# Kernel optimization log

Measured on AMD Instinct MI355X. Metric: run time of the kernel, lower is better.

## Reference

```python
import jax, jax.numpy as jnp
import numpy as np

N = 50000
E = 800000
D_IN = 256
D_H = 256


def setup_inputs() -> dict:
    key = jax.random.key(0)
    ks = jax.random.split(key, 8)
    x = jax.random.normal(ks[0], (N, D_IN), dtype=jnp.float32)
    W1 = jax.random.normal(ks[1], (D_H, D_IN), dtype=jnp.float32) * (1.0 / np.sqrt(D_IN))
    b1 = jnp.zeros((D_H,), dtype=jnp.float32)
    W2 = jax.random.normal(ks[2], (D_H, D_H), dtype=jnp.float32) * (1.0 / np.sqrt(D_H))
    b2 = jnp.zeros((D_H,), dtype=jnp.float32)
    gamma = jnp.ones((D_H,), dtype=jnp.float32)
    beta = jnp.zeros((D_H,), dtype=jnp.float32)
    adj_values = jax.random.uniform(ks[3], (E,), dtype=jnp.float32)
    rows = jax.random.randint(ks[4], (E,), 0, N, dtype=jnp.int64)
    cols = jax.random.randint(ks[5], (E,), 0, N, dtype=jnp.int64)
    adj_indices = jnp.stack([rows, cols], axis=0)
    return {"x": x, "W1": W1, "b1": b1, "W2": W2, "b2": b2,
            "gamma": gamma, "beta": beta, "adj_values": adj_values,
            "adj_indices": adj_indices}


def _spmm(adj_indices, adj_values, h, n):
    # out[i] = sum_j A[i, j] * h[j]; COO row=indices[0], col=indices[1]
    rows, cols = adj_indices[0], adj_indices[1]
    msgs = adj_values[:, None] * h[cols]          # [E, D]
    return jax.ops.segment_sum(msgs, rows, num_segments=n)


def _layernorm(h, gamma, beta, eps=1e-5):
    mu = jnp.mean(h, axis=-1, keepdims=True)
    var = jnp.var(h, axis=-1, keepdims=True)
    return (h - mu) * jax.lax.rsqrt(var + eps) * gamma + beta


def reference(x, W1, b1, W2, b2, gamma, beta, adj_values, adj_indices):
    n = x.shape[0]
    h = x @ W1.T + b1
    h = _spmm(adj_indices, adj_values, h, n)
    h = jax.nn.gelu(h, approximate=False)
    h = h @ W2.T + b2
    h = _spmm(adj_indices, adj_values, h, n)
    h = jax.nn.gelu(h, approximate=False)
    h = _layernorm(h + x[:, :h.shape[1]], gamma, beta)
    return h
```

## Files before the change

### kernel.cpp

```cpp
#include <hip/hip_runtime.h>
#include <math.h>

#define DH 256
#define CAP 64

typedef _Float16 f16x4 __attribute__((ext_vector_type(4)));
typedef _Float16 f16x8 __attribute__((ext_vector_type(8)));
typedef __fp16 fp16x2 __attribute__((ext_vector_type(2)));
typedef float f32x4 __attribute__((ext_vector_type(4)));

__device__ __forceinline__ float gelu_exact(float v) {
    return 0.5f * v * (1.0f + erff(v * 0.70710678118654752f));
}

__device__ __forceinline__ unsigned short f2h_bits(float f) {
    _Float16 h = (_Float16)f;
    return __builtin_bit_cast(unsigned short, h);
}

__device__ __forceinline__ _Float16 bits2h(unsigned short u) {
    return __builtin_bit_cast(_Float16, u);
}

__device__ __forceinline__ unsigned pk2h(float a, float b) {
    fp16x2 r = __builtin_amdgcn_cvt_pkrtz(a, b);
    return __builtin_bit_cast(unsigned, r);
}

__device__ __forceinline__ void async_copy16(const void* g, void* l) {
    __builtin_amdgcn_global_load_lds(
        (const __attribute__((address_space(1))) void*)g,
        (__attribute__((address_space(3))) void*)l, 16, 0, 0);
}

__global__ void prep_kernel(const float* __restrict__ W1, const float* __restrict__ W2,
                            unsigned short* __restrict__ W1h, unsigned short* __restrict__ W2h,
                            int* __restrict__ cnt, int n) {
    const int WV = DH * DH / 4;
    int gid = blockIdx.x * blockDim.x + threadIdx.x;
    if (gid < 2 * WV) {
        const float* src = (gid < WV) ? W1 : W2;
        unsigned short* dst = (gid < WV) ? W1h : W2h;
        int i = (gid < WV) ? gid : gid - WV;
        float4 v = *(const float4*)(src + (size_t)i * 4);
        uint2 o;
        o.x = pk2h(v.x, v.y);
        o.y = pk2h(v.z, v.w);
        *(uint2*)(dst + (size_t)i * 4) = o;
    } else {
        int i = (gid - 2 * WV) * 4;
        if (i < n) {
            int4 z = {0, 0, 0, 0};
            if (i + 4 <= n) *(int4*)(cnt + i) = z;
            else for (int k = i; k < n; ++k) cnt[k] = 0;
        }
    }
}

__global__ void bucket_kernel(const int* __restrict__ idx, const float* __restrict__ vals,
                              int* __restrict__ cnt, unsigned* __restrict__ cvb, int E) {
    int e = blockIdx.x * blockDim.x + threadIdx.x;
    if (e >= E) return;
    int r = idx[e];
    int c = idx[E + e];
    float v = vals[e];
    int p = atomicAdd(&cnt[r], 1);
    if (p < CAP) {
        cvb[(size_t)r * CAP + p] = ((unsigned)c << 16) | (unsigned)f2h_bits(v);
    }
}

template<bool AF32>
__global__ __launch_bounds__(512) void gemm_mfma_kernel(
        const void* __restrict__ Ap, const unsigned short* __restrict__ B,
        const float* __restrict__ bias, unsigned short* __restrict__ C, int M) {
    __shared__ char smem[49152];
    char* sA = smem;
    char* sB = smem + 16384;
    const int tid  = threadIdx.x;
    const int lane = tid & 63;
    const int wid  = tid >> 6;
    const int m0   = blockIdx.x * 128;
    const int wm   = wid >> 2;
    const int wn   = wid & 3;
    const int l15  = lane & 15, l4 = lane >> 4;

    auto stage = [&](int k0) {
        #pragma unroll
        for (int k = 0; k < 2; ++k) {
            int t = k * 512 + tid;
            int row = t >> 3;
            int sw  = (t & 7) ^ (row & 7);
            int gra = m0 + row; if (gra >= M) gra = M - 1;
            if (AF32) {
                const float* a32 = (const float*)Ap + (size_t)gra * DH + k0 + sw * 8;
                float4 lo = *(const float4*)a32;
                float4 hi = *(const float4*)(a32 + 4);
                uint4 pk;
                pk.x = pk2h(lo.x, lo.y);
                pk.y = pk2h(lo.z, lo.w);
                pk.z = pk2h(hi.x, hi.y);
                pk.w = pk2h(hi.z, hi.w);
                *(uint4*)(sA + (size_t)t * 16) = pk;
            } else {
                async_copy16((const unsigned short*)Ap + (size_t)gra * DH + k0 + sw * 8,
                             sA + ((size_t)(k * 512 + wid * 64)) * 16);
            }
        }
        #pragma unroll
        for (int k = 0; k < 4; ++k) {
            int t = k * 512 + tid;
            int row = t >> 3;
            int sw  = (t & 7) ^ (row & 7);
            async_copy16(B + (size_t)row * DH + k0 + sw * 8,
                         sB + ((size_t)(k * 512 + wid * 64)) * 16);
        }
    };

    f32x4 acc[4][4] = {};

    stage(0);
    __syncthreads();

    #pragma unroll
    for (int t = 0; t < 4; ++t) {
        f16x8 af[4][2], bfg[4][2];
        #pragma unroll
        for (int f = 0; f < 4; ++f) {
            int ra = wm * 64 + f * 16 + l15;
            int rb = wn * 64 + f * 16 + l15;
            #pragma unroll
            for (int kf = 0; kf < 2; ++kf) {
                int ca = ((kf * 4 + l4) ^ (ra & 7)) * 16;
                int cb = ((kf * 4 + l4) ^ (rb & 7)) * 16;
                af[f][kf]  = *(const f16x8*)(sA + ra * 128 + ca);
                bfg[f][kf] = *(const f16x8*)(sB + rb * 128 + cb);
            }
        }
        #pragma unroll
        for (int fm = 0; fm < 4; ++fm)
            #pragma unroll
            for (int fn = 0; fn < 4; ++fn) {
                acc[fm][fn] = __builtin_amdgcn_mfma_f32_16x16x32_f16(af[fm][0], bfg[fn][0], acc[fm][fn], 0, 0, 0);
                acc[fm][fn] = __builtin_amdgcn_mfma_f32_16x16x32_f16(af[fm][1], bfg[fn][1], acc[fm][fn], 0, 0, 0);
            }
        if (t < 3) {
            __syncthreads();
            stage((t + 1) * 64);
            __syncthreads();
        }
    }

    #pragma unroll
    for (int fn = 0; fn < 4; ++fn) {
        float bb = bias[wn * 64 + fn * 16 + l15];
        #pragma unroll
        for (int fm = 0; fm < 4; ++fm) {
            int mrow = m0 + wm * 64 + fm * 16 + l4 * 4;
            unsigned short* cp = C + (size_t)mrow * DH + wn * 64 + fn * 16 + l15;
            #pragma unroll
            for (int r = 0; r < 4; ++r) {
                if (mrow + r < M) cp[(size_t)r * DH] = f2h_bits(acc[fm][fn][r] + bb);
            }
        }
    }
}

template<int MODE>
__global__ __launch_bounds__(256) void spmm_kernel(
        const _Float16* __restrict__ h, const int* __restrict__ cnt,
        const unsigned* __restrict__ cvb, const float* __restrict__ xres,
        const float* __restrict__ gamma, const float* __restrict__ beta,
        void* __restrict__ outp, int n) {
    const int lane = threadIdx.x & 63;
    const int row = blockIdx.x * 4 + (threadIdx.x >> 6);
    if (row >= n) return;
    int deg = cnt[row]; if (deg > CAP) deg = CAP;
    const unsigned* cb = cvb + (size_t)row * CAP;

    f16x4 accA = {}, accB = {};
    int j = 0;
    for (; j + 4 <= deg; j += 4) {
        uint4 e = *(const uint4*)(cb + j);
        f16x4 p0 = *(const f16x4*)(h + (size_t)(e.x >> 16) * DH + lane * 4);
        f16x4 p1 = *(const f16x4*)(h + (size_t)(e.y >> 16) * DH + lane * 4);
        f16x4 p2 = *(const f16x4*)(h + (size_t)(e.z >> 16) * DH + lane * 4);
        f16x4 p3 = *(const f16x4*)(h + (size_t)(e.w >> 16) * DH + lane * 4);
        _Float16 v0 = bits2h((unsigned short)(e.x & 0xFFFFu));
        _Float16 v1 = bits2h((unsigned short)(e.y & 0xFFFFu));
        _Float16 v2 = bits2h((unsigned short)(e.z & 0xFFFFu));
        _Float16 v3 = bits2h((unsigned short)(e.w & 0xFFFFu));
        accA += p0 * v0; accB += p1 * v1;
        accA += p2 * v2; accB += p3 * v3;
    }
    for (; j < deg; ++j) {
        unsigned e = cb[j];
        f16x4 p0 = *(const f16x4*)(h + (size_t)(e >> 16) * DH + lane * 4);
        _Float16 v0 = bits2h((unsigned short)(e & 0xFFFFu));
        accA += p0 * v0;
    }

    float ax = (float)accA[0] + (float)accB[0];
    float ay = (float)accA[1] + (float)accB[1];
    float az = (float)accA[2] + (float)accB[2];
    float aw = (float)accA[3] + (float)accB[3];

    ax = gelu_exact(ax); ay = gelu_exact(ay); az = gelu_exact(az); aw = gelu_exact(aw);

    if (MODE == 1) {
        float4 xr = *(const float4*)(xres + (size_t)row * DH + lane * 4);
        ax += xr.x; ay += xr.y; az += xr.z; aw += xr.w;
        float s  = ax + ay + az + aw;
        float s2 = ax * ax + ay * ay + az * az + aw * aw;
        #pragma unroll
        for (int off = 32; off > 0; off >>= 1) {
            s  += __shfl_xor(s,  off);
            s2 += __shfl_xor(s2, off);
        }
        float mu  = s * (1.0f / 256.0f);
        float var = s2 * (1.0f / 256.0f) - mu * mu;
        float rs  = rsqrtf(var + 1e-5f);
        float4 g  = *(const float4*)(gamma + lane * 4);
        float4 bt = *(const float4*)(beta + lane * 4);
        float4 o;
        o.x = (ax - mu) * rs * g.x + bt.x;
        o.y = (ay - mu) * rs * g.y + bt.y;
        o.z = (az - mu) * rs * g.z + bt.z;
        o.w = (aw - mu) * rs * g.w + bt.w;
        *(float4*)((float*)outp + (size_t)row * DH + lane * 4) = o;
    } else {
        uint2 pk;
        pk.x = pk2h(ax, ay);
        pk.y = pk2h(az, aw);
        *(uint2*)((_Float16*)outp + (size_t)row * DH + lane * 4) = pk;
    }
}

extern "C" void kernel_launch(void* const* d_in, const int* in_sizes, int n_in,
                              void* d_out, int out_size, void* d_ws, size_t ws_size,
                              hipStream_t stream) {
    const float* x     = (const float*)d_in[0];
    const float* W1    = (const float*)d_in[1];
    const float* b1    = (const float*)d_in[2];
    const float* W2    = (const float*)d_in[3];
    const float* b2    = (const float*)d_in[4];
    const float* gamma = (const float*)d_in[5];
    const float* beta  = (const float*)d_in[6];
    const float* avals = (const float*)d_in[7];
    const int*   aidx  = (const int*)d_in[8];

    const int n = in_sizes[0] / DH;
    const int e = in_sizes[7];
    float* out = (float*)d_out;

    _Float16* g1h = (_Float16*)d_out;

    char* ws = (char*)d_ws;
    size_t off = 0;
    _Float16* hb = (_Float16*)(ws + off);              off += (size_t)n * DH * 2;
    off = (off + 255) & ~(size_t)255;
    unsigned short* W1h = (unsigned short*)(ws + off); off += (size_t)DH * DH * 2;
    off = (off + 255) & ~(size_t)255;
    unsigned short* W2h = (unsigned short*)(ws + off); off += (size_t)DH * DH * 2;
    off = (off + 255) & ~(size_t)255;
    int* cnt = (int*)(ws + off);                       off += (size_t)n * sizeof(int);
    off = (off + 255) & ~(size_t)255;
    unsigned* cvb = (unsigned*)(ws + off);             off += (size_t)n * CAP * sizeof(unsigned);

    const int gemm_gx = (n + 127) / 128;
    const int prep_items = 2 * (DH * DH / 4) + (n + 3) / 4;

    prep_kernel<<<(prep_items + 255) / 256, 256, 0, stream>>>(W1, W2, W1h, W2h, cnt, n);
    bucket_kernel<<<(e + 255) / 256, 256, 0, stream>>>(aidx, avals, cnt, cvb, e);

    gemm_mfma_kernel<true><<<gemm_gx, 512, 0, stream>>>(x, W1h, b1, (unsigned short*)hb, n);

    spmm_kernel<0><<<(n + 3) / 4, 256, 0, stream>>>(
        hb, cnt, cvb, nullptr, nullptr, nullptr, g1h, n);

    gemm_mfma_kernel<false><<<gemm_gx, 512, 0, stream>>>(g1h, W2h, b2, (unsigned short*)hb, n);

    spmm_kernel<1><<<(n + 3) / 4, 256, 0, stream>>>(
        hb, cnt, cvb, x, gamma, beta, out, n);
}
```

Measured before the change: 229.8 us.

## Double-buffer GEMM shared-memory K tiles with halved K step

Restructures the MFMA GEMM main loop to use two shared-memory buffers with a K-step of 32 instead of a single buffer with a K-step of 64. The next tile's loads are issued before computing on the current tile, so global-to-LDS traffic overlaps the MFMA work and each iteration needs only one barrier instead of two. The trade-off is twice as many iterations, each with half the MFMA work between barriers, and a narrower 4-way XOR swizzle that may raise LDS bank conflicts.

```diff
diff --git a/kernel.cpp b/kernel.cpp
--- a/kernel.cpp
+++ b/kernel.cpp
@@ -75,8 +75,6 @@
         const void* __restrict__ Ap, const unsigned short* __restrict__ B,
         const float* __restrict__ bias, unsigned short* __restrict__ C, int M) {
     __shared__ char smem[49152];
-    char* sA = smem;
-    char* sB = smem + 16384;
     const int tid  = threadIdx.x;
     const int lane = tid & 63;
     const int wid  = tid >> 6;
@@ -85,12 +83,13 @@
     const int wn   = wid & 3;
     const int l15  = lane & 15, l4 = lane >> 4;
 
-    auto stage = [&](int k0) {
-        #pragma unroll
-        for (int k = 0; k < 2; ++k) {
-            int t = k * 512 + tid;
-            int row = t >> 3;
-            int sw  = (t & 7) ^ (row & 7);
+    auto stage = [&](int buf, int k0) {
+        char* sA = smem + buf * 24576;
+        char* sB = sA + 8192;
+        {
+            int t = tid;
+            int row = t >> 2;
+            int sw  = (t & 3) ^ (row & 3);
             int gra = m0 + row; if (gra >= M) gra = M - 1;
             if (AF32) {
                 const float* a32 = (const float*)Ap + (size_t)gra * DH + k0 + sw * 8;
@@ -104,14 +103,14 @@
                 *(uint4*)(sA + (size_t)t * 16) = pk;
             } else {
                 async_copy16((const unsigned short*)Ap + (size_t)gra * DH + k0 + sw * 8,
-                             sA + ((size_t)(k * 512 + wid * 64)) * 16);
+                             sA + ((size_t)(wid * 64)) * 16);
             }
         }
         #pragma unroll
-        for (int k = 0; k < 4; ++k) {
+        for (int k = 0; k < 2; ++k) {
             int t = k * 512 + tid;
-            int row = t >> 3;
-            int sw  = (t & 7) ^ (row & 7);
+            int row = t >> 2;
+            int sw  = (t & 3) ^ (row & 3);
             async_copy16(B + (size_t)row * DH + k0 + sw * 8,
                          sB + ((size_t)(k * 512 + wid * 64)) * 16);
         }
@@ -119,36 +118,32 @@
 
     f32x4 acc[4][4] = {};
 
-    stage(0);
+    stage(0, 0);
     __syncthreads();
 
     #pragma unroll
-    for (int t = 0; t < 4; ++t) {
-        f16x8 af[4][2], bfg[4][2];
+    for (int t = 0; t < 8; ++t) {
+        if (t < 7) stage((t + 1) & 1, (t + 1) * 32);
+
+        char* sA = smem + (t & 1) * 24576;
+        char* sB = sA + 8192;
+        f16x8 af[4], bfg[4];
         #pragma unroll
         for (int f = 0; f < 4; ++f) {
             int ra = wm * 64 + f * 16 + l15;
             int rb = wn * 64 + f * 16 + l15;
-            #pragma unroll
-            for (int kf = 0; kf < 2; ++kf) {
-                int ca = ((kf * 4 + l4) ^ (ra & 7)) * 16;
-                int cb = ((kf * 4 + l4) ^ (rb & 7)) * 16;
-                af[f][kf]  = *(const f16x8*)(sA + ra * 128 + ca);
-                bfg[f][kf] = *(const f16x8*)(sB + rb * 128 + cb);
-            }
+            int ca = (l4 ^ (ra & 3)) * 16;
+            int cb = (l4 ^ (rb & 3)) * 16;
+            af[f]  = *(const f16x8*)(sA + ra * 64 + ca);
+            bfg[f] = *(const f16x8*)(sB + rb * 64 + cb);
         }
         #pragma unroll
         for (int fm = 0; fm < 4; ++fm)
             #pragma unroll
-            for (int fn = 0; fn < 4; ++fn) {
-                acc[fm][fn] = __builtin_amdgcn_mfma_f32_16x16x32_f16(af[fm][0], bfg[fn][0], acc[fm][fn], 0, 0, 0);
-                acc[fm][fn] = __builtin_amdgcn_mfma_f32_16x16x32_f16(af[fm][1], bfg[fn][1], acc[fm][fn], 0, 0, 0);
-            }
-        if (t < 3) {
-            __syncthreads();
-            stage((t + 1) * 64);
-            __syncthreads();
-        }
+            for (int fn = 0; fn < 4; ++fn)
+                acc[fm][fn] = __builtin_amdgcn_mfma_f32_16x16x32_f16(af[fm], bfg[fn], acc[fm][fn], 0, 0, 0);
+
+        __syncthreads();
     }
 
     #pragma unroll
```

Result: faster. 216.2 us (-5.9%).
